# Performance work log

Measured on AMD Instinct MI355X. Metric: run time of the kernel, lower is better.

## Reference

```python
import jax, jax.numpy as jnp
import numpy as np

F_DIM = 256
N_HEADS = 4
D_Q = F_DIM // N_HEADS  # 64
EPS = 1e-6


def layer_norm(x, g, b):
    mu = jnp.mean(x, axis=-1, keepdims=True)
    var = jnp.mean(jnp.square(x - mu), axis=-1, keepdims=True)
    return (x - mu) * jax.lax.rsqrt(var + EPS) * g + b


def linear(x, W, b):
    # torch nn.Linear: y = x @ W.T + b, W: [out, in]
    return jnp.einsum('...i,oi->...o', x, W) + b


def setup_inputs() -> dict:
    key = jax.random.key(0)
    ks = jax.random.split(key, 16)
    f = F_DIM
    inp = {
        'code_map': jax.random.normal(ks[0], (8, 512, f), jnp.float32),
        'texture_map': jax.random.normal(ks[1], (8, 512, f), jnp.float32),
        'Wq': jax.random.normal(ks[2], (N_HEADS * D_Q, f), jnp.float32) * 0.02,
        'bq': jnp.zeros((N_HEADS * D_Q,), jnp.float32),
        'Wk': jax.random.normal(ks[3], (N_HEADS * D_Q, f), jnp.float32) * 0.02,
        'bk': jnp.zeros((N_HEADS * D_Q,), jnp.float32),
        'Wv': jax.random.normal(ks[4], (N_HEADS * D_Q, f), jnp.float32) * 0.02,
        'bv': jnp.zeros((N_HEADS * D_Q,), jnp.float32),
        'Wo': jax.random.normal(ks[5], (f, N_HEADS * D_Q), jnp.float32) * 0.02,
        'bo': jnp.zeros((f,), jnp.float32),
        'ln1_g': jnp.ones((f,), jnp.float32), 'ln1_b': jnp.zeros((f,), jnp.float32),
        'ln2_g': jnp.ones((f,), jnp.float32), 'ln2_b': jnp.zeros((f,), jnp.float32),
        'ffln_g': jnp.ones((f,), jnp.float32), 'ffln_b': jnp.zeros((f,), jnp.float32),
        'W1': jax.random.normal(ks[6], (f, f), jnp.float32) * 0.02,
        'b1': jnp.zeros((f,), jnp.float32),
        'W2': jax.random.normal(ks[7], (f, f), jnp.float32) * 0.02,
        'b2': jnp.zeros((f,), jnp.float32),
    }
    return inp


def reference(code_map, texture_map, Wq, bq, Wk, bk, Wv, bv, Wo, bo,
              ln1_g, ln1_b, ln2_g, ln2_b, ffln_g, ffln_b, W1, b1, W2, b2):
    n_code, V, f = code_map.shape
    bs = texture_map.shape[0]
    h, dq = N_HEADS, D_Q

    # LayerNorms (code side -> ln1, texture side -> ln2); expansion via repeat
    # is a pure broadcast, so keep code side [n_code,...] and texture side [bs,...].
    code2 = layer_norm(code_map, ln1_g, ln1_b)       # [n, V, f]
    tex2 = layer_norm(texture_map, ln2_g, ln2_b)     # [b, V, f]

    q = linear(tex2, Wq, bq).reshape(bs, V, h, dq)    # [b, V, h, d]
    k = linear(code2, Wk, bk).reshape(n_code, V, h, dq)
    v = linear(code2, Wv, bv).reshape(n_code, V, h, dq)

    scale = 1.0 / jnp.sqrt(jnp.asarray(dq, q.dtype))
    # scores: [b, n, h, Vq, Vk]
    scores = jnp.einsum('bqhd,nkhd->bnhqk', q, k) * scale
    attn = jax.nn.softmax(scores, axis=-1)
    ctx = jnp.einsum('bnhqk,nkhd->bnhqd', attn, v)    # [b, n, h, V, d]
    ctx = ctx.transpose(0, 1, 3, 2, 4).reshape(bs, n_code, V, h * dq)
    feat = linear(ctx, Wo, bo)                        # [b, n, V, f]

    x = texture_map[:, None, :, :] + feat             # residual with broadcast
    # ffR: MLP_res_block
    y = layer_norm(x, ffln_g, ffln_b)
    y = linear(jax.nn.relu(linear(y, W1, b1)), W2, b2)
    return x + y
```

## Files before the change

### kernel.cpp

```cpp
#include <hip/hip_runtime.h>
#include <hip/hip_bf16.h>

#define F 256
#define V 512
#define NB 8
#define NC 8
#define NH 4
#define DQ 64
#define EPS 1e-6f

typedef __hip_bfloat16 bf16;
typedef __attribute__((ext_vector_type(8))) short short8;
typedef __attribute__((ext_vector_type(4))) float f32x4;
typedef __attribute__((ext_vector_type(4))) unsigned uint4v;

__device__ __forceinline__ float b2f(bf16 x){ return __bfloat162float(x); }
__device__ __forceinline__ float shf(short s){
    return __bfloat162float(__builtin_bit_cast(bf16, (unsigned short)s));
}

#define MFMA(a,b,c) __builtin_amdgcn_mfma_f32_16x16x32_bf16((a),(b),(c),0,0,0)

__device__ __forceinline__ unsigned pack2bf(float a, float b){
    unsigned short ua = __builtin_bit_cast(unsigned short, __float2bfloat16(a));
    unsigned short ub = __builtin_bit_cast(unsigned short, __float2bfloat16(b));
    return (unsigned)ua | ((unsigned)ub << 16);
}

__global__ void castw_kernel(const float* __restrict__ w0, const float* __restrict__ w1,
                             const float* __restrict__ w2, const float* __restrict__ w3,
                             const float* __restrict__ w4, const float* __restrict__ w5,
                             bf16* __restrict__ dst){
    int which = blockIdx.x >> 8;
    int idx = ((blockIdx.x & 255) << 8) | threadIdx.x;
    const float* s = which==0?w0: which==1?w1: which==2?w2: which==3?w3: which==4?w4: w5;
    dst[which * (F*F) + idx] = __float2bfloat16(s[idx]);
}

__global__ void ln_kernel(const float* __restrict__ code, const float* __restrict__ tex,
                          const float* __restrict__ ln1_g, const float* __restrict__ ln1_b,
                          const float* __restrict__ ln2_g, const float* __restrict__ ln2_b,
                          bf16* __restrict__ cn, bf16* __restrict__ tn, bf16* __restrict__ tb){
    __shared__ float red[256];
    int r = blockIdx.x, t = threadIdx.x;
    int is_tex = r >> 12;
    int row = r & 4095;
    const float* src = is_tex ? tex : code;
    const float* g   = is_tex ? ln2_g : ln1_g;
    const float* be  = is_tex ? ln2_b : ln1_b;
    bf16* dst        = is_tex ? tn : cn;

    float x = src[row * F + t];
    if (is_tex) tb[row * F + t] = __float2bfloat16(x);
    red[t] = x; __syncthreads();
    for(int s2 = 128; s2 > 0; s2 >>= 1){ if(t < s2) red[t] += red[t + s2]; __syncthreads(); }
    float mu = red[0] * (1.0f / F); __syncthreads();
    float d = x - mu;
    red[t] = d * d; __syncthreads();
    for(int s2 = 128; s2 > 0; s2 >>= 1){ if(t < s2) red[t] += red[t + s2]; __syncthreads(); }
    float rs = rsqrtf(red[0] * (1.0f / F) + EPS);
    dst[row * F + t] = __float2bfloat16(d * rs * g[t] + be[t]);
}

__global__ __launch_bounds__(256) void qkvgemm_kernel(const bf16* __restrict__ cn,
                                                      const bf16* __restrict__ tn,
                                                      const bf16* __restrict__ wbf,
                                                      const float* __restrict__ bq,
                                                      const float* __restrict__ bk,
                                                      const float* __restrict__ bv,
                                                      bf16* __restrict__ qn,
                                                      bf16* __restrict__ k4,
                                                      bf16* __restrict__ v4){
    int which = blockIdx.z;
    const bf16* in   = (which == 0) ? tn : cn;
    const bf16* wb   = wbf + which * (F * F);
    const float* bias = (which == 0) ? bq : (which == 1) ? bk : bv;

    int w = threadIdx.x >> 6, lane = threadIdx.x & 63;
    int lg = lane >> 4, li = lane & 15;
    int rowbase = blockIdx.x * 128 + w * 32;
    int colbase = blockIdx.y * 64;

    f32x4 acc[2][4];
    #pragma unroll
    for(int mi = 0; mi < 2; mi++)
        #pragma unroll
        for(int ni = 0; ni < 4; ni++) acc[mi][ni] = (f32x4){0.f,0.f,0.f,0.f};

    #pragma unroll
    for(int kc = 0; kc < 8; kc++){
        short8 a[2], bb[4];
        #pragma unroll
        for(int mi = 0; mi < 2; mi++)
            a[mi] = *(const short8*)(in + (rowbase + mi * 16 + li) * F + kc * 32 + lg * 8);
        #pragma unroll
        for(int ni = 0; ni < 4; ni++)
            bb[ni] = *(const short8*)(wb + (colbase + ni * 16 + li) * F + kc * 32 + lg * 8);
        #pragma unroll
        for(int mi = 0; mi < 2; mi++)
            #pragma unroll
            for(int ni = 0; ni < 4; ni++)
                acc[mi][ni] = MFMA(a[mi], bb[ni], acc[mi][ni]);
    }

    #pragma unroll
    for(int mi = 0; mi < 2; mi++){
        #pragma unroll
        for(int r = 0; r < 4; r++){
            int row = rowbase + mi * 16 + lg * 4 + r;
            #pragma unroll
            for(int ni = 0; ni < 4; ni++){
                int col = colbase + ni * 16 + li;
                float val = acc[mi][ni][r] + bias[col];
                if (which == 0)
                    qn[row * F + col] = __float2bfloat16(val);
                else if (which == 1){
                    int n = row >> 9, keyl = row & (V - 1);
                    int kc2 = keyl >> 5, kt = (keyl >> 4) & 1, lip = keyl & 15;
                    int hh = col >> 6, ks = (col >> 5) & 1, lgp = (col >> 3) & 3, j = col & 7;
                    int fi = ((n * 16 + kc2) * 2 + kt) * 8 + hh * 2 + ks;
                    k4[fi * 512 + lgp * 128 + lip * 8 + j] = __float2bfloat16(val);
                } else {
                    int n = row >> 9, key = row & (V - 1);
                    v4[(((n * 16 + (key >> 5)) * F) + col) * 32 + (key & 31)] = __float2bfloat16(val);
                }
            }
        }
    }
}

__global__ __launch_bounds__(512, 4) void attn_mlp_kernel(const bf16* __restrict__ qn,
                                                          const bf16* __restrict__ k4,
                                                          const bf16* __restrict__ v4,
                                                          const bf16* __restrict__ wbf,
                                                          const float* __restrict__ bo,
                                                          const bf16* __restrict__ tb,
                                                          const float* __restrict__ ffg,
                                                          const float* __restrict__ ffb,
                                                          const float* __restrict__ b1,
                                                          const float* __restrict__ b2,
                                                          float* __restrict__ out){
    __shared__ bf16 xs[32][264];
    __shared__ float red[512], red2[512];
    __shared__ float stat[32][2];
    int n = blockIdx.x & 7, b = blockIdx.x >> 3, qt = blockIdx.y;
    int tid = threadIdx.x;
    int w = tid >> 6, lane = tid & 63;
    int h = w & 3, qh = w >> 2;
    int lg = lane >> 4, li = lane & 15;

    short8 qB[2];
    #pragma unroll
    for(int ks = 0; ks < 2; ks++)
        qB[ks] = *(const short8*)(qn + (b * V + qt * 32 + qh * 16 + li) * F
                                     + h * DQ + ks * 32 + lg * 8);

    f32x4 o[4];
    #pragma unroll
    for(int dt = 0; dt < 4; dt++) o[dt] = (f32x4){0.f,0.f,0.f,0.f};
    float l_acc = 0.f;

    const float scale = 0.125f;
    int g1 = lg & 1;
    int lhA = li | ((2 * g1) << 4);
    int lhB = lhA | 16;
    bool hi = lane >= 32;
    int fel = lg * 128 + li * 8;

    short8 kA0, kA1, kA2, kA3, vA0, vA1, vA2, vA3;
    {
        int fb = ((n * 16 + 0) * 2) * 8 + h * 2;
        kA0 = *(const short8*)(k4 + (fb + 0) * 512 + fel);
        kA1 = *(const short8*)(k4 + (fb + 1) * 512 + fel);
        kA2 = *(const short8*)(k4 + (fb + 8) * 512 + fel);
        kA3 = *(const short8*)(k4 + (fb + 9) * 512 + fel);
        const bf16* vb = v4 + ((n * 16 + 0) * F + h * DQ) * 32;
        vA0 = *(const short8*)(vb + (0 * 16 + li) * 32 + lg * 8);
        vA1 = *(const short8*)(vb + (1 * 16 + li) * 32 + lg * 8);
        vA2 = *(const short8*)(vb + (2 * 16 + li) * 32 + lg * 8);
        vA3 = *(const short8*)(vb + (3 * 16 + li) * 32 + lg * 8);
    }

    #pragma unroll
    for(int kc = 0; kc < 16; kc++){
        short8 nk0, nk1, nk2, nk3, nv0, nv1, nv2, nv3;
        if (kc < 15){
            int fb = ((n * 16 + kc + 1) * 2) * 8 + h * 2;
            nk0 = *(const short8*)(k4 + (fb + 0) * 512 + fel);
            nk1 = *(const short8*)(k4 + (fb + 1) * 512 + fel);
            nk2 = *(const short8*)(k4 + (fb + 8) * 512 + fel);
            nk3 = *(const short8*)(k4 + (fb + 9) * 512 + fel);
            const bf16* vb = v4 + ((n * 16 + kc + 1) * F + h * DQ) * 32;
            nv0 = *(const short8*)(vb + (0 * 16 + li) * 32 + lg * 8);
            nv1 = *(const short8*)(vb + (1 * 16 + li) * 32 + lg * 8);
            nv2 = *(const short8*)(vb + (2 * 16 + li) * 32 + lg * 8);
            nv3 = *(const short8*)(vb + (3 * 16 + li) * 32 + lg * 8);
        }

        f32x4 st0 = (f32x4){0.f,0.f,0.f,0.f};
        f32x4 st1 = (f32x4){0.f,0.f,0.f,0.f};
        st0 = MFMA(kA0, qB[0], st0);
        st1 = MFMA(kA2, qB[0], st1);
        st0 = MFMA(kA1, qB[1], st0);
        st1 = MFMA(kA3, qB[1], st1);

        float p[2][4], rsum = 0.f;
        #pragma unroll
        for(int r = 0; r < 4; r++){
            p[0][r] = __expf(st0[r] * scale);
            p[1][r] = __expf(st1[r] * scale);
            rsum += p[0][r] + p[1][r];
        }
        l_acc += rsum;

        unsigned pk00 = pack2bf(p[0][0], p[0][1]);
        unsigned pk01 = pack2bf(p[0][2], p[0][3]);
        unsigned pk10 = pack2bf(p[1][0], p[1][1]);
        unsigned pk11 = pack2bf(p[1][2], p[1][3]);

        unsigned d0a = __shfl((int)pk00, lhA, 64);
        unsigned d0b = __shfl((int)pk10, lhA, 64);
        unsigned d1a = __shfl((int)pk01, lhA, 64);
        unsigned d1b = __shfl((int)pk11, lhA, 64);
        unsigned d2a = __shfl((int)pk00, lhB, 64);
        unsigned d2b = __shfl((int)pk10, lhB, 64);
        unsigned d3a = __shfl((int)pk01, lhB, 64);
        unsigned d3b = __shfl((int)pk11, lhB, 64);
        uint4v uv;
        uv.x = hi ? d0b : d0a;
        uv.y = hi ? d1b : d1a;
        uv.z = hi ? d2b : d2a;
        uv.w = hi ? d3b : d3a;
        short8 pfrag = __builtin_bit_cast(short8, uv);

        o[0] = MFMA(vA0, pfrag, o[0]);
        o[1] = MFMA(vA1, pfrag, o[1]);
        o[2] = MFMA(vA2, pfrag, o[2]);
        o[3] = MFMA(vA3, pfrag, o[3]);

        kA0 = nk0; kA1 = nk1; kA2 = nk2; kA3 = nk3;
        vA0 = nv0; vA1 = nv1; vA2 = nv2; vA3 = nv3;
    }

    l_acc += __shfl_xor(l_acc, 16);
    l_acc += __shfl_xor(l_acc, 32);
    float inv = 1.0f / l_acc;

    #pragma unroll
    for(int dt = 0; dt < 4; dt++){
        uint2 pkd;
        pkd.x = pack2bf(o[dt][0] * inv, o[dt][1] * inv);
        pkd.y = pack2bf(o[dt][2] * inv, o[dt][3] * inv);
        *(uint2*)&xs[qh * 16 + li][h * DQ + dt * 16 + lg * 4] = pkd;
    }
    __syncthreads();

    const bf16* Wo = wbf + 3 * (F * F);
    int colbase = w * 32;
    f32x4 xac[2][2];
    #pragma unroll
    for(int mi = 0; mi < 2; mi++)
        #pragma unroll
        for(int ni = 0; ni < 2; ni++) xac[mi][ni] = (f32x4){0.f,0.f,0.f,0.f};
    #pragma unroll
    for(int kc = 0; kc < 8; kc++){
        short8 a0 = *(const short8*)&xs[li][kc * 32 + lg * 8];
        short8 a1 = *(const short8*)&xs[16 + li][kc * 32 + lg * 8];
        #pragma unroll
        for(int ni = 0; ni < 2; ni++){
            short8 bw = *(const short8*)(Wo + (colbase + ni * 16 + li) * F + kc * 32 + lg * 8);
            xac[0][ni] = MFMA(a0, bw, xac[0][ni]);
            xac[1][ni] = MFMA(a1, bw, xac[1][ni]);
        }
    }
    float xres[2][2][4];
    #pragma unroll
    for(int mi = 0; mi < 2; mi++)
        #pragma unroll
        for(int r = 0; r < 4; r++){
            int qrel = mi * 16 + lg * 4 + r;
            #pragma unroll
            for(int ni = 0; ni < 2; ni++){
                int col = colbase + ni * 16 + li;
                xres[mi][ni][r] = xac[mi][ni][r] + bo[col]
                                + b2f(tb[(b * V + qt * 32 + qrel) * F + col]);
            }
        }
    __syncthreads();
    #pragma unroll
    for(int mi = 0; mi < 2; mi++)
        #pragma unroll
        for(int r = 0; r < 4; r++){
            int qrel = mi * 16 + lg * 4 + r;
            #pragma unroll
            for(int ni = 0; ni < 2; ni++)
                xs[qrel][colbase + ni * 16 + li] = __float2bfloat16(xres[mi][ni][r]);
        }
    __syncthreads();

    int row = tid >> 4, sub = tid & 15;
    short8 xa = *(const short8*)&xs[row][sub * 16];
    short8 xb2 = *(const short8*)&xs[row][sub * 16 + 8];
    float sum = 0.f, sq = 0.f;
    #pragma unroll
    for(int j = 0; j < 8; j++){
        float v0 = shf(xa[j]), v1 = shf(xb2[j]);
        sum += v0 + v1; sq += v0 * v0 + v1 * v1;
    }
    red[tid] = sum; red2[tid] = sq;
    __syncthreads();
    if (tid < 32){
        float s = 0.f, q2 = 0.f;
        #pragma unroll
        for(int i = 0; i < 16; i++){ s += red[tid * 16 + i]; q2 += red2[tid * 16 + i]; }
        float mu = s * (1.0f / F);
        float var = q2 * (1.0f / F) - mu * mu;
        stat[tid][0] = mu;
        stat[tid][1] = rsqrtf(var + EPS);
    }
    __syncthreads();
    {
        float mu = stat[row][0], rsv = stat[row][1];
        float nv[16];
        #pragma unroll
        for(int j = 0; j < 8; j++){
            int c0 = sub * 16 + j, c1 = sub * 16 + 8 + j;
            nv[j]     = (shf(xa[j])  - mu) * rsv * ffg[c0] + ffb[c0];
            nv[8 + j] = (shf(xb2[j]) - mu) * rsv * ffg[c1] + ffb[c1];
        }
        uint4v pa, pb;
        pa.x = pack2bf(nv[0], nv[1]);  pa.y = pack2bf(nv[2], nv[3]);
        pa.z = pack2bf(nv[4], nv[5]);  pa.w = pack2bf(nv[6], nv[7]);
        pb.x = pack2bf(nv[8], nv[9]);  pb.y = pack2bf(nv[10], nv[11]);
        pb.z = pack2bf(nv[12], nv[13]); pb.w = pack2bf(nv[14], nv[15]);
        *(short8*)&xs[row][sub * 16]     = __builtin_bit_cast(short8, pa);
        *(short8*)&xs[row][sub * 16 + 8] = __builtin_bit_cast(short8, pb);
    }
    __syncthreads();

    const bf16* W1b = wbf + 4 * (F * F);
    f32x4 hac[2][2];
    #pragma unroll
    for(int mi = 0; mi < 2; mi++)
        #pragma unroll
        for(int ni = 0; ni < 2; ni++) hac[mi][ni] = (f32x4){0.f,0.f,0.f,0.f};
    #pragma unroll
    for(int kc = 0; kc < 8; kc++){
        short8 a0 = *(const short8*)&xs[li][kc * 32 + lg * 8];
        short8 a1 = *(const short8*)&xs[16 + li][kc * 32 + lg * 8];
        #pragma unroll
        for(int ni = 0; ni < 2; ni++){
            short8 bw = *(const short8*)(W1b + (colbase + ni * 16 + li) * F + kc * 32 + lg * 8);
            hac[0][ni] = MFMA(a0, bw, hac[0][ni]);
            hac[1][ni] = MFMA(a1, bw, hac[1][ni]);
        }
    }
    __syncthreads();
    #pragma unroll
    for(int mi = 0; mi < 2; mi++)
        #pragma unroll
        for(int r = 0; r < 4; r++){
            int rr = mi * 16 + lg * 4 + r;
            #pragma unroll
            for(int ni = 0; ni < 2; ni++){
                int col = colbase + ni * 16 + li;
                xs[rr][col] = __float2bfloat16(fmaxf(hac[mi][ni][r] + b1[col], 0.f));
            }
        }
    __syncthreads();

    const bf16* W2b = wbf + 5 * (F * F);
    f32x4 oac[2][2];
    #pragma unroll
    for(int mi = 0; mi < 2; mi++)
        #pragma unroll
        for(int ni = 0; ni < 2; ni++) oac[mi][ni] = (f32x4){0.f,0.f,0.f,0.f};
    #pragma unroll
    for(int kc = 0; kc < 8; kc++){
        short8 a0 = *(const short8*)&xs[li][kc * 32 + lg * 8];
        short8 a1 = *(const short8*)&xs[16 + li][kc * 32 + lg * 8];
        #pragma unroll
        for(int ni = 0; ni < 2; ni++){
            short8 bw = *(const short8*)(W2b + (colbase + ni * 16 + li) * F + kc * 32 + lg * 8);
            oac[0][ni] = MFMA(a0, bw, oac[0][ni]);
            oac[1][ni] = MFMA(a1, bw, oac[1][ni]);
        }
    }
    #pragma unroll
    for(int mi = 0; mi < 2; mi++)
        #pragma unroll
        for(int r = 0; r < 4; r++){
            int qrel = mi * 16 + lg * 4 + r;
            int ro = (b * NC + n) * V + qt * 32 + qrel;
            #pragma unroll
            for(int ni = 0; ni < 2; ni++){
                int col = colbase + ni * 16 + li;
                out[ro * F + col] = oac[mi][ni][r] + b2[col] + xres[mi][ni][r];
            }
        }
}

extern "C" void kernel_launch(void* const* d_in, const int* in_sizes, int n_in,
                              void* d_out, int out_size, void* d_ws, size_t ws_size,
                              hipStream_t stream) {
    const float* code_map = (const float*)d_in[0];
    const float* tex_map  = (const float*)d_in[1];
    const float* Wq = (const float*)d_in[2];  const float* bq = (const float*)d_in[3];
    const float* Wk = (const float*)d_in[4];  const float* bk = (const float*)d_in[5];
    const float* Wv = (const float*)d_in[6];  const float* bv = (const float*)d_in[7];
    const float* Wo = (const float*)d_in[8];  const float* bo = (const float*)d_in[9];
    const float* ln1_g = (const float*)d_in[10]; const float* ln1_b = (const float*)d_in[11];
    const float* ln2_g = (const float*)d_in[12]; const float* ln2_b = (const float*)d_in[13];
    const float* ffln_g = (const float*)d_in[14]; const float* ffln_b = (const float*)d_in[15];
    const float* W1 = (const float*)d_in[16]; const float* b1 = (const float*)d_in[17];
    const float* W2 = (const float*)d_in[18]; const float* b2 = (const float*)d_in[19];
    float* out = (float*)d_out;

    bf16* ws  = (bf16*)d_ws;
    bf16* qn  = ws;
    bf16* k4  = qn + 1048576;
    bf16* v4  = k4 + 1048576;
    bf16* cn  = v4 + 1048576;
    bf16* tn  = cn + 1048576;
    bf16* tb  = tn + 1048576;
    bf16* wbf = tb + 1048576;

    castw_kernel<<<6 * 256, 256, 0, stream>>>(Wq, Wk, Wv, Wo, W1, W2, wbf);
    ln_kernel<<<8192, 256, 0, stream>>>(code_map, tex_map, ln1_g, ln1_b, ln2_g, ln2_b, cn, tn, tb);
    qkvgemm_kernel<<<dim3(32, 4, 3), 256, 0, stream>>>(cn, tn, wbf, bq, bk, bv, qn, k4, v4);
    attn_mlp_kernel<<<dim3(64, 16), 512, 0, stream>>>(qn, k4, v4, wbf, bo, tb,
                                                      ffln_g, ffln_b, b1, b2, out);
}
```

Before: 227.7 us.

## Vectorize LN and cast, stage QKV epilogue in LDS, double-buffer attention loads

Several changes land together. The weight cast and the LayerNorm now use float4 loads, and LayerNorm computes one row per wavefront with shuffle reductions in place of the shared-memory tree. The QKV GEMM uses smaller tiles and stages its output through LDS so stores are coalesced, and K is now written row-major instead of in a scattered fragment layout. The attention loop prefetches K/V two chunks ahead and raises wave priority around the MFMAs. The three MLP GEMMs double-buffer their weight fragments and load the residual early. Register pressure rises, and the new K layout may make K loads in attention less contiguous.

New measurement: 268.4 us. +17.9%, slower.

```diff
diff --git a/kernel.cpp b/kernel.cpp
--- a/kernel.cpp
+++ b/kernel.cpp
@@ -31,18 +31,21 @@
                              const float* __restrict__ w2, const float* __restrict__ w3,
                              const float* __restrict__ w4, const float* __restrict__ w5,
                              bf16* __restrict__ dst){
-    int which = blockIdx.x >> 8;
-    int idx = ((blockIdx.x & 255) << 8) | threadIdx.x;
+    int which = blockIdx.x >> 6;
+    int idx = (((blockIdx.x & 63) << 8) | threadIdx.x) << 2;
     const float* s = which==0?w0: which==1?w1: which==2?w2: which==3?w3: which==4?w4: w5;
-    dst[which * (F*F) + idx] = __float2bfloat16(s[idx]);
-}
-
-__global__ void ln_kernel(const float* __restrict__ code, const float* __restrict__ tex,
+    float4 v = *(const float4*)(s + idx);
+    uint2 p; p.x = pack2bf(v.x, v.y); p.y = pack2bf(v.z, v.w);
+    *(uint2*)(dst + which * (F*F) + idx) = p;
+}
+
+__global__ __launch_bounds__(256) void ln_kernel(const float* __restrict__ code,
+                          const float* __restrict__ tex,
                           const float* __restrict__ ln1_g, const float* __restrict__ ln1_b,
                           const float* __restrict__ ln2_g, const float* __restrict__ ln2_b,
                           bf16* __restrict__ cn, bf16* __restrict__ tn, bf16* __restrict__ tb){
-    __shared__ float red[256];
-    int r = blockIdx.x, t = threadIdx.x;
+    int w = threadIdx.x >> 6, lane = threadIdx.x & 63;
+    int r = blockIdx.x * 4 + w;
     int is_tex = r >> 12;
     int row = r & 4095;
     const float* src = is_tex ? tex : code;
@@ -50,96 +53,114 @@
     const float* be  = is_tex ? ln2_b : ln1_b;
     bf16* dst        = is_tex ? tn : cn;
 
-    float x = src[row * F + t];
-    if (is_tex) tb[row * F + t] = __float2bfloat16(x);
-    red[t] = x; __syncthreads();
-    for(int s2 = 128; s2 > 0; s2 >>= 1){ if(t < s2) red[t] += red[t + s2]; __syncthreads(); }
-    float mu = red[0] * (1.0f / F); __syncthreads();
-    float d = x - mu;
-    red[t] = d * d; __syncthreads();
-    for(int s2 = 128; s2 > 0; s2 >>= 1){ if(t < s2) red[t] += red[t + s2]; __syncthreads(); }
-    float rs = rsqrtf(red[0] * (1.0f / F) + EPS);
-    dst[row * F + t] = __float2bfloat16(d * rs * g[t] + be[t]);
-}
-
-__global__ __launch_bounds__(256) void qkvgemm_kernel(const bf16* __restrict__ cn,
-                                                      const bf16* __restrict__ tn,
-                                                      const bf16* __restrict__ wbf,
-                                                      const float* __restrict__ bq,
-                                                      const float* __restrict__ bk,
-                                                      const float* __restrict__ bv,
-                                                      bf16* __restrict__ qn,
-                                                      bf16* __restrict__ k4,
-                                                      bf16* __restrict__ v4){
+    float4 x = *(const float4*)(src + row * F + lane * 4);
+    if (is_tex){
+        uint2 p; p.x = pack2bf(x.x, x.y); p.y = pack2bf(x.z, x.w);
+        *(uint2*)(tb + row * F + lane * 4) = p;
+    }
+    float s = x.x + x.y + x.z + x.w;
+    #pragma unroll
+    for(int m = 1; m < 64; m <<= 1) s += __shfl_xor(s, m);
+    float mu = s * (1.0f / F);
+    float d0 = x.x - mu, d1 = x.y - mu, d2 = x.z - mu, d3 = x.w - mu;
+    float q = d0*d0 + d1*d1 + d2*d2 + d3*d3;
+    #pragma unroll
+    for(int m = 1; m < 64; m <<= 1) q += __shfl_xor(q, m);
+    float rs = rsqrtf(q * (1.0f / F) + EPS);
+    float4 gg = *(const float4*)(g + lane * 4);
+    float4 bb = *(const float4*)(be + lane * 4);
+    uint2 p;
+    p.x = pack2bf(d0 * rs * gg.x + bb.x, d1 * rs * gg.y + bb.y);
+    p.y = pack2bf(d2 * rs * gg.z + bb.z, d3 * rs * gg.w + bb.w);
+    *(uint2*)(dst + row * F + lane * 4) = p;
+}
+
+__global__ __launch_bounds__(256) __attribute__((amdgpu_waves_per_eu(2,3)))
+void qkv_kernel(const bf16* __restrict__ cn,
+                const bf16* __restrict__ tn,
+                const bf16* __restrict__ wbf,
+                const float* __restrict__ bq,
+                const float* __restrict__ bk,
+                const float* __restrict__ bv,
+                bf16* __restrict__ qn,
+                bf16* __restrict__ kn,
+                bf16* __restrict__ v4){
+    __shared__ bf16 ts[64][72];
     int which = blockIdx.z;
     const bf16* in   = (which == 0) ? tn : cn;
     const bf16* wb   = wbf + which * (F * F);
     const float* bias = (which == 0) ? bq : (which == 1) ? bk : bv;
 
-    int w = threadIdx.x >> 6, lane = threadIdx.x & 63;
+    int tid = threadIdx.x;
+    int w = tid >> 6, lane = tid & 63;
     int lg = lane >> 4, li = lane & 15;
-    int rowbase = blockIdx.x * 128 + w * 32;
+    int rowbase = blockIdx.x * 64 + w * 16;
     int colbase = blockIdx.y * 64;
 
-    f32x4 acc[2][4];
-    #pragma unroll
-    for(int mi = 0; mi < 2; mi++)
-        #pragma unroll
-        for(int ni = 0; ni < 4; ni++) acc[mi][ni] = (f32x4){0.f,0.f,0.f,0.f};
+    f32x4 acc[4];
+    #pragma unroll
+    for(int ni = 0; ni < 4; ni++) acc[ni] = (f32x4){0.f,0.f,0.f,0.f};
+
+    const bf16* arow = in + (rowbase + li) * F + lg * 8;
+    const bf16* brow = wb + (colbase + li) * F + lg * 8;
 
     #pragma unroll
     for(int kc = 0; kc < 8; kc++){
-        short8 a[2], bb[4];
-        #pragma unroll
-        for(int mi = 0; mi < 2; mi++)
-            a[mi] = *(const short8*)(in + (rowbase + mi * 16 + li) * F + kc * 32 + lg * 8);
+        short8 a = *(const short8*)(arow + kc * 32);
+        #pragma unroll
+        for(int ni = 0; ni < 4; ni++){
+            short8 bbf = *(const short8*)(brow + ni * 16 * F + kc * 32);
+            acc[ni] = MFMA(a, bbf, acc[ni]);
+        }
+    }
+
+    if (which < 2){
         #pragma unroll
         for(int ni = 0; ni < 4; ni++)
-            bb[ni] = *(const short8*)(wb + (colbase + ni * 16 + li) * F + kc * 32 + lg * 8);
-        #pragma unroll
-        for(int mi = 0; mi < 2; mi++)
-            #pragma unroll
-            for(int ni = 0; ni < 4; ni++)
-                acc[mi][ni] = MFMA(a[mi], bb[ni], acc[mi][ni]);
-    }
-
-    #pragma unroll
-    for(int mi = 0; mi < 2; mi++){
-        #pragma unroll
-        for(int r = 0; r < 4; r++){
-            int row = rowbase + mi * 16 + lg * 4 + r;
-            #pragma unroll
-            for(int ni = 0; ni < 4; ni++){
-                int col = colbase + ni * 16 + li;
-                float val = acc[mi][ni][r] + bias[col];
-                if (which == 0)
-                    qn[row * F + col] = __float2bfloat16(val);
-                else if (which == 1){
-                    int n = row >> 9, keyl = row & (V - 1);
-                    int kc2 = keyl >> 5, kt = (keyl >> 4) & 1, lip = keyl & 15;
-                    int hh = col >> 6, ks = (col >> 5) & 1, lgp = (col >> 3) & 3, j = col & 7;
-                    int fi = ((n * 16 + kc2) * 2 + kt) * 8 + hh * 2 + ks;
-                    k4[fi * 512 + lgp * 128 + lip * 8 + j] = __float2bfloat16(val);
-                } else {
-                    int n = row >> 9, key = row & (V - 1);
-                    v4[(((n * 16 + (key >> 5)) * F) + col) * 32 + (key & 31)] = __float2bfloat16(val);
-                }
-            }
-        }
-    }
-}
-
-__global__ __launch_bounds__(512, 4) void attn_mlp_kernel(const bf16* __restrict__ qn,
-                                                          const bf16* __restrict__ k4,
-                                                          const bf16* __restrict__ v4,
-                                                          const bf16* __restrict__ wbf,
-                                                          const float* __restrict__ bo,
-                                                          const bf16* __restrict__ tb,
-                                                          const float* __restrict__ ffg,
-                                                          const float* __restrict__ ffb,
-                                                          const float* __restrict__ b1,
-                                                          const float* __restrict__ b2,
-                                                          float* __restrict__ out){
+            #pragma unroll
+            for(int r = 0; r < 4; r++)
+                ts[w * 16 + lg * 4 + r][ni * 16 + li] =
+                    __float2bfloat16(acc[ni][r] + bias[colbase + ni * 16 + li]);
+    } else {
+        #pragma unroll
+        for(int ni = 0; ni < 4; ni++)
+            #pragma unroll
+            for(int r = 0; r < 4; r++)
+                ts[ni * 16 + li][w * 16 + lg * 4 + r] =
+                    __float2bfloat16(acc[ni][r] + bias[colbase + ni * 16 + li]);
+    }
+    __syncthreads();
+
+    if (which < 2){
+        bf16* outp = which ? kn : qn;
+        int rr = tid >> 2, gg2 = tid & 3;
+        *(short8*)(outp + (blockIdx.x * 64 + rr) * F + colbase + gg2 * 16)
+            = *(const short8*)&ts[rr][gg2 * 16];
+    } else {
+        int col = tid & 63, half = tid >> 6;
+        int keybase = blockIdx.x * 64;
+        int n = keybase >> 9;
+        int keyl = (keybase & (V - 1)) + half * 16;
+        int chunk = keyl >> 5, off = keyl & 31;
+        *(short8*)(v4 + ((n * 16 + chunk) * F + colbase + col) * 32 + off)
+            = *(const short8*)&ts[col][half * 16];
+    }
+}
+
+#define BLOAD(Wp, kcc, nii) (*(const short8*)((Wp) + (colbase + (nii)*16 + li) * F + (kcc) * 32 + lg * 8))
+
+__global__ __launch_bounds__(512, 4) __attribute__((amdgpu_waves_per_eu(4,4)))
+void attn_mlp_kernel(const bf16* __restrict__ qn,
+                     const bf16* __restrict__ kn,
+                     const bf16* __restrict__ v4,
+                     const bf16* __restrict__ wbf,
+                     const float* __restrict__ bo,
+                     const bf16* __restrict__ tb,
+                     const float* __restrict__ ffg,
+                     const float* __restrict__ ffb,
+                     const float* __restrict__ b1,
+                     const float* __restrict__ b2,
+                     float* __restrict__ out){
     __shared__ bf16 xs[32][264];
     __shared__ float red[512], red2[512];
     __shared__ float stat[32][2];
@@ -165,44 +186,40 @@
     int lhA = li | ((2 * g1) << 4);
     int lhB = lhA | 16;
     bool hi = lane >= 32;
-    int fel = lg * 128 + li * 8;
-
-    short8 kA0, kA1, kA2, kA3, vA0, vA1, vA2, vA3;
-    {
-        int fb = ((n * 16 + 0) * 2) * 8 + h * 2;
-        kA0 = *(const short8*)(k4 + (fb + 0) * 512 + fel);
-        kA1 = *(const short8*)(k4 + (fb + 1) * 512 + fel);
-        kA2 = *(const short8*)(k4 + (fb + 8) * 512 + fel);
-        kA3 = *(const short8*)(k4 + (fb + 9) * 512 + fel);
-        const bf16* vb = v4 + ((n * 16 + 0) * F + h * DQ) * 32;
-        vA0 = *(const short8*)(vb + (0 * 16 + li) * 32 + lg * 8);
-        vA1 = *(const short8*)(vb + (1 * 16 + li) * 32 + lg * 8);
-        vA2 = *(const short8*)(vb + (2 * 16 + li) * 32 + lg * 8);
-        vA3 = *(const short8*)(vb + (3 * 16 + li) * 32 + lg * 8);
+
+    const bf16* kb_ = kn + (n * V + li) * F + h * DQ + lg * 8;
+    const bf16* vb_ = v4 + (n * 16 * F + h * DQ) * 32 + li * 32 + lg * 8;
+
+    short8 kbuf[2][4], vbuf[2][4];
+    #pragma unroll
+    for(int c = 0; c < 2; c++){
+        kbuf[c][0] = *(const short8*)(kb_ + (c * 32 +  0) * F);
+        kbuf[c][1] = *(const short8*)(kb_ + (c * 32 +  0) * F + 32);
+        kbuf[c][2] = *(const short8*)(kb_ + (c * 32 + 16) * F);
+        kbuf[c][3] = *(const short8*)(kb_ + (c * 32 + 16) * F + 32);
+        vbuf[c][0] = *(const short8*)(vb_ + (c * F +  0) * 32);
+        vbuf[c][1] = *(const short8*)(vb_ + (c * F + 16) * 32);
+        vbuf[c][2] = *(const short8*)(vb_ + (c * F + 32) * 32);
+        vbuf[c][3] = *(const short8*)(vb_ + (c * F + 48) * 32);
     }
 
     #pragma unroll
     for(int kc = 0; kc < 16; kc++){
-        short8 nk0, nk1, nk2, nk3, nv0, nv1, nv2, nv3;
-        if (kc < 15){
-            int fb = ((n * 16 + kc + 1) * 2) * 8 + h * 2;
-            nk0 = *(const short8*)(k4 + (fb + 0) * 512 + fel);
-            nk1 = *(const short8*)(k4 + (fb + 1) * 512 + fel);
-            nk2 = *(const short8*)(k4 + (fb + 8) * 512 + fel);
-            nk3 = *(const short8*)(k4 + (fb + 9) * 512 + fel);
-            const bf16* vb = v4 + ((n * 16 + kc + 1) * F + h * DQ) * 32;
-            nv0 = *(const short8*)(vb + (0 * 16 + li) * 32 + lg * 8);
-            nv1 = *(const short8*)(vb + (1 * 16 + li) * 32 + lg * 8);
-            nv2 = *(const short8*)(vb + (2 * 16 + li) * 32 + lg * 8);
-            nv3 = *(const short8*)(vb + (3 * 16 + li) * 32 + lg * 8);
-        }
-
+        const int cur = kc & 1;
         f32x4 st0 = (f32x4){0.f,0.f,0.f,0.f};
         f32x4 st1 = (f32x4){0.f,0.f,0.f,0.f};
-        st0 = MFMA(kA0, qB[0], st0);
-        st1 = MFMA(kA2, qB[0], st1);
-        st0 = MFMA(kA1, qB[1], st0);
-        st1 = MFMA(kA3, qB[1], st1);
+        __builtin_amdgcn_s_setprio(1);
+        st0 = MFMA(kbuf[cur][0], qB[0], st0);
+        st1 = MFMA(kbuf[cur][2], qB[0], st1);
+        st0 = MFMA(kbuf[cur][1], qB[1], st0);
+        st1 = MFMA(kbuf[cur][3], qB[1], st1);
+        __builtin_amdgcn_s_setprio(0);
+        if (kc < 14){
+            kbuf[cur][0] = *(const short8*)(kb_ + ((kc + 2) * 32 +  0) * F);
+            kbuf[cur][1] = *(const short8*)(kb_ + ((kc + 2) * 32 +  0) * F + 32);
+            kbuf[cur][2] = *(const short8*)(kb_ + ((kc + 2) * 32 + 16) * F);
+            kbuf[cur][3] = *(const short8*)(kb_ + ((kc + 2) * 32 + 16) * F + 32);
+        }
 
         float p[2][4], rsum = 0.f;
         #pragma unroll
@@ -233,13 +250,18 @@
         uv.w = hi ? d3b : d3a;
         short8 pfrag = __builtin_bit_cast(short8, uv);
 
-        o[0] = MFMA(vA0, pfrag, o[0]);
-        o[1] = MFMA(vA1, pfrag, o[1]);
-        o[2] = MFMA(vA2, pfrag, o[2]);
-        o[3] = MFMA(vA3, pfrag, o[3]);
-
-        kA0 = nk0; kA1 = nk1; kA2 = nk2; kA3 = nk3;
-        vA0 = nv0; vA1 = nv1; vA2 = nv2; vA3 = nv3;
+        __builtin_amdgcn_s_setprio(1);
+        o[0] = MFMA(vbuf[cur][0], pfrag, o[0]);
+        o[1] = MFMA(vbuf[cur][1], pfrag, o[1]);
+        o[2] = MFMA(vbuf[cur][2], pfrag, o[2]);
+        o[3] = MFMA(vbuf[cur][3], pfrag, o[3]);
+        __builtin_amdgcn_s_setprio(0);
+        if (kc < 14){
+            vbuf[cur][0] = *(const short8*)(vb_ + ((kc + 2) * F +  0) * 32);
+            vbuf[cur][1] = *(const short8*)(vb_ + ((kc + 2) * F + 16) * 32);
+            vbuf[cur][2] = *(const short8*)(vb_ + ((kc + 2) * F + 32) * 32);
+            vbuf[cur][3] = *(const short8*)(vb_ + ((kc + 2) * F + 48) * 32);
+        }
     }
 
     l_acc += __shfl_xor(l_acc, 16);
@@ -253,24 +275,42 @@
         pkd.y = pack2bf(o[dt][2] * inv, o[dt][3] * inv);
         *(uint2*)&xs[qh * 16 + li][h * DQ + dt * 16 + lg * 4] = pkd;
     }
+
+    int colbase = w * 32;
+    float tres[2][2][4];
+    #pragma unroll
+    for(int mi = 0; mi < 2; mi++)
+        #pragma unroll
+        for(int r = 0; r < 4; r++){
+            int qrel = mi * 16 + lg * 4 + r;
+            #pragma unroll
+            for(int ni = 0; ni < 2; ni++)
+                tres[mi][ni][r] = b2f(tb[(b * V + qt * 32 + qrel) * F + colbase + ni * 16 + li]);
+        }
     __syncthreads();
 
     const bf16* Wo = wbf + 3 * (F * F);
-    int colbase = w * 32;
     f32x4 xac[2][2];
     #pragma unroll
     for(int mi = 0; mi < 2; mi++)
         #pragma unroll
         for(int ni = 0; ni < 2; ni++) xac[mi][ni] = (f32x4){0.f,0.f,0.f,0.f};
-    #pragma unroll
-    for(int kc = 0; kc < 8; kc++){
-        short8 a0 = *(const short8*)&xs[li][kc * 32 + lg * 8];
-        short8 a1 = *(const short8*)&xs[16 + li][kc * 32 + lg * 8];
-        #pragma unroll
-        for(int ni = 0; ni < 2; ni++){
-            short8 bw = *(const short8*)(Wo + (colbase + ni * 16 + li) * F + kc * 32 + lg * 8);
-            xac[0][ni] = MFMA(a0, bw, xac[0][ni]);
-            xac[1][ni] = MFMA(a1, bw, xac[1][ni]);
+    {
+        short8 bw[2][2];
+        bw[0][0] = BLOAD(Wo, 0, 0); bw[0][1] = BLOAD(Wo, 0, 1);
+        bw[1][0] = BLOAD(Wo, 1, 0); bw[1][1] = BLOAD(Wo, 1, 1);
+        #pragma unroll
+        for(int kc = 0; kc < 8; kc++){
+            short8 a0 = *(const short8*)&xs[li][kc * 32 + lg * 8];
+            short8 a1 = *(const short8*)&xs[16 + li][kc * 32 + lg * 8];
+            xac[0][0] = MFMA(a0, bw[kc & 1][0], xac[0][0]);
+            xac[1][0] = MFMA(a1, bw[kc & 1][0], xac[1][0]);
+            xac[0][1] = MFMA(a0, bw[kc & 1][1], xac[0][1]);
+            xac[1][1] = MFMA(a1, bw[kc & 1][1], xac[1][1]);
+            if (kc < 6){
+                bw[kc & 1][0] = BLOAD(Wo, kc + 2, 0);
+                bw[kc & 1][1] = BLOAD(Wo, kc + 2, 1);
+            }
         }
     }
     float xres[2][2][4];
@@ -278,12 +318,10 @@
     for(int mi = 0; mi < 2; mi++)
         #pragma unroll
         for(int r = 0; r < 4; r++){
-            int qrel = mi * 16 + lg * 4 + r;
             #pragma unroll
             for(int ni = 0; ni < 2; ni++){
                 int col = colbase + ni * 16 + li;
-                xres[mi][ni][r] = xac[mi][ni][r] + bo[col]
-                                + b2f(tb[(b * V + qt * 32 + qrel) * F + col]);
+                xres[mi][ni][r] = xac[mi][ni][r] + bo[col] + tres[mi][ni][r];
             }
         }
     __syncthreads();
@@ -344,15 +382,22 @@
     for(int mi = 0; mi < 2; mi++)
         #pragma unroll
         for(int ni = 0; ni < 2; ni++) hac[mi][ni] = (f32x4){0.f,0.f,0.f,0.f};
-    #pragma unroll
-    for(int kc = 0; kc < 8; kc++){
-        short8 a0 = *(const short8*)&xs[li][kc * 32 + lg * 8];
-        short8 a1 = *(const short8*)&xs[16 + li][kc * 32 + lg * 8];
-        #pragma unroll
-        for(int ni = 0; ni < 2; ni++){
-            short8 bw = *(const short8*)(W1b + (colbase + ni * 16 + li) * F + kc * 32 + lg * 8);
-            hac[0][ni] = MFMA(a0, bw, hac[0][ni]);
-            hac[1][ni] = MFMA(a1, bw, hac[1][ni]);
+    {
+        short8 bw[2][2];
+        bw[0][0] = BLOAD(W1b, 0, 0); bw[0][1] = BLOAD(W1b, 0, 1);
+        bw[1][0] = BLOAD(W1b, 1, 0); bw[1][1] = BLOAD(W1b, 1, 1);
+        #pragma unroll
+        for(int kc = 0; kc < 8; kc++){
+            short8 a0 = *(const short8*)&xs[li][kc * 32 + lg * 8];
+            short8 a1 = *(const short8*)&xs[16 + li][kc * 32 + lg * 8];
+            hac[0][0] = MFMA(a0, bw[kc & 1][0], hac[0][0]);
+            hac[1][0] = MFMA(a1, bw[kc & 1][0], hac[1][0]);
+            hac[0][1] = MFMA(a0, bw[kc & 1][1], hac[0][1]);
+            hac[1][1] = MFMA(a1, bw[kc & 1][1], hac[1][1]);
+            if (kc < 6){
+                bw[kc & 1][0] = BLOAD(W1b, kc + 2, 0);
+                bw[kc & 1][1] = BLOAD(W1b, kc + 2, 1);
+            }
         }
     }
     __syncthreads();
@@ -375,15 +420,22 @@
     for(int mi = 0; mi < 2; mi++)
         #pragma unroll
         for(int ni = 0; ni < 2; ni++) oac[mi][ni] = (f32x4){0.f,0.f,0.f,0.f};
-    #pragma unroll
-    for(int kc = 0; kc < 8; kc++){
-        short8 a0 = *(const short8*)&xs[li][kc * 32 + lg * 8];
-        short8 a1 = *(const short8*)&xs[16 + li][kc * 32 + lg * 8];
-        #pragma unroll
-        for(int ni = 0; ni < 2; ni++){
-            short8 bw = *(const short8*)(W2b + (colbase + ni * 16 + li) * F + kc * 32 + lg * 8);
-            oac[0][ni] = MFMA(a0, bw, oac[0][ni]);
-            oac[1][ni] = MFMA(a1, bw, oac[1][ni]);
+    {
+        short8 bw[2][2];
+        bw[0][0] = BLOAD(W2b, 0, 0); bw[0][1] = BLOAD(W2b, 0, 1);
+        bw[1][0] = BLOAD(W2b, 1, 0); bw[1][1] = BLOAD(W2b, 1, 1);
+        #pragma unroll
+        for(int kc = 0; kc < 8; kc++){
+            short8 a0 = *(const short8*)&xs[li][kc * 32 + lg * 8];
+            short8 a1 = *(const short8*)&xs[16 + li][kc * 32 + lg * 8];
+            oac[0][0] = MFMA(a0, bw[kc & 1][0], oac[0][0]);
+            oac[1][0] = MFMA(a1, bw[kc & 1][0], oac[1][0]);
+            oac[0][1] = MFMA(a0, bw[kc & 1][1], oac[0][1]);
+            oac[1][1] = MFMA(a1, bw[kc & 1][1], oac[1][1]);
+            if (kc < 6){
+                bw[kc & 1][0] = BLOAD(W2b, kc + 2, 0);
+                bw[kc & 1][1] = BLOAD(W2b, kc + 2, 1);
+            }
         }
     }
     #pragma unroll
@@ -418,16 +470,16 @@
 
     bf16* ws  = (bf16*)d_ws;
     bf16* qn  = ws;
-    bf16* k4  = qn + 1048576;
-    bf16* v4  = k4 + 1048576;
+    bf16* kn  = qn + 1048576;
+    bf16* v4  = kn + 1048576;
     bf16* cn  = v4 + 1048576;
     bf16* tn  = cn + 1048576;
     bf16* tb  = tn + 1048576;
     bf16* wbf = tb + 1048576;
 
-    castw_kernel<<<6 * 256, 256, 0, stream>>>(Wq, Wk, Wv, Wo, W1, W2, wbf);
-    ln_kernel<<<8192, 256, 0, stream>>>(code_map, tex_map, ln1_g, ln1_b, ln2_g, ln2_b, cn, tn, tb);
-    qkvgemm_kernel<<<dim3(32, 4, 3), 256, 0, stream>>>(cn, tn, wbf, bq, bk, bv, qn, k4, v4);
-    attn_mlp_kernel<<<dim3(64, 16), 512, 0, stream>>>(qn, k4, v4, wbf, bo, tb,
+    castw_kernel<<<6 * 64, 256, 0, stream>>>(Wq, Wk, Wv, Wo, W1, W2, wbf);
+    ln_kernel<<<2048, 256, 0, stream>>>(code_map, tex_map, ln1_g, ln1_b, ln2_g, ln2_b, cn, tn, tb);
+    qkv_kernel<<<dim3(64, 4, 3), 256, 0, stream>>>(cn, tn, wbf, bq, bk, bv, qn, kn, v4);
+    attn_mlp_kernel<<<dim3(64, 16), 512, 0, stream>>>(qn, kn, v4, wbf, bo, tb,
                                                       ffln_g, ffln_b, b1, b2, out);
 }
```
